# Kernel tuning notes

Measured on AMD Instinct MI355X. Metric: run time of the kernel, lower is better.

## Reference

```python
import jax, jax.numpy as jnp
import numpy as np

B, C, G, Q, OUT = 2, 96, 32, 32, 45
M_FREQS = 12
SIGMA = 3.0


def _fourier_encode(c):
    # c: [..., 3]; log-linear frequency bank scaled by SIGMA (sigma**(j/m))
    m = M_FREQS
    freqs = SIGMA ** (jnp.arange(m, dtype=c.dtype) / m)          # [m]
    ang = 2.0 * jnp.pi * c[..., None] * freqs                    # [..., 3, m]
    enc = jnp.concatenate([jnp.sin(ang), jnp.cos(ang)], axis=-1)  # [..., 3, 2m]
    return enc.reshape(c.shape[:-1] + (3 * 2 * m,))


def setup_inputs():
    key = jax.random.key(0)
    ks = jax.random.split(key, 10)
    d = {}
    d["context_v"] = jax.random.normal(ks[0], (B, C, G, G, G), jnp.float32)
    g = jnp.arange(G, dtype=jnp.float32)
    grid = jnp.stack(jnp.meshgrid(g, g, g, indexing="ij"), axis=-1)  # [G,G,G,3]
    d["context_world_coord_grid"] = jnp.broadcast_to(grid, (B, G, G, G, 3))
    # queries strictly inside the grid so floor()+1 <= G-1
    d["query_world_coord"] = jax.random.uniform(ks[1], (B, Q, Q, Q, 3), jnp.float32, 0.0, G - 1.001)
    d["query_world_coord_mask"] = jnp.ones((B, Q, Q, Q, 1), dtype=bool)
    eye = jnp.broadcast_to(jnp.eye(4, dtype=jnp.float32), (B, 4, 4))
    d["affine_context_vox2world"] = eye
    d["affine_query_vox2world"] = eye
    d["context_vox_size_world"] = jnp.ones((B, 3), jnp.float32)
    d["query_vox_size_world"] = jnp.ones((B, 3), jnp.float32)

    n_coord = 6 + 3 * 2 * M_FREQS  # 78
    internal = C + n_coord         # 174

    def lin(k, fi, fo):
        s = 1.0 / np.sqrt(fi)
        kw, kb = jax.random.split(k)
        return (jax.random.uniform(kw, (fi, fo), jnp.float32, -s, s),
                jax.random.uniform(kb, (fo,), jnp.float32, -s, s))

    pk = jax.random.split(ks[2], 7)
    d["w00"], d["b00"] = lin(pk[0], internal, C)
    d["w01"], d["b01"] = lin(pk[1], C, C)
    d["w02"], d["b02"] = lin(pk[2], C, C)
    d["w10"], d["b10"] = lin(pk[3], internal, C)
    d["w11"], d["b11"] = lin(pk[4], C, C)
    d["w12"], d["b12"] = lin(pk[5], C, C)
    d["w_post"], d["b_post"] = lin(pk[6], C, OUT)
    return d


def reference(context_v, context_world_coord_grid, query_world_coord,
              query_world_coord_mask, affine_context_vox2world,
              affine_query_vox2world, context_vox_size_world,
              query_vox_size_world, w00, b00, w01, b01, w02, b02,
              w10, b10, w11, b11, w12, b12, w_post, b_post):
    Bq = context_v.shape[0]
    qshape = query_world_coord.shape
    qw = query_world_coord.reshape(Bq, -1, 3)          # [B,N,3]
    N = qw.shape[1]
    qm = query_world_coord_mask.reshape(Bq, -1, 1)     # [B,N,1]
    dummy = qw[:, N // 2][:, None]                      # [B,1,3]
    qw = jnp.where(qm, qw, dummy)

    inv = jnp.linalg.inv(affine_context_vox2world)
    q_vox = jnp.einsum("brc,bnc->bnr", inv[:, :3, :3], qw) + inv[:, None, :3, 3]
    bottom = jnp.floor(q_vox).astype(jnp.int32)         # [B,N,3]
    sub = q_vox - bottom.astype(q_vox.dtype)

    cvt = jnp.transpose(context_v, (0, 2, 3, 4, 1))     # [B,X,Y,Z,C]
    bidx = jnp.arange(Bq)[:, None]
    maskf = qm.astype(q_vox.dtype)
    blocks = ((w00, b00, w01, b01, w02, b02), (w10, b10, w11, b11, w12, b12))
    acc = jnp.zeros((Bq, N, w_post.shape[1]), q_vox.dtype)

    for oi in (0, 1):
        for oj in (0, 1):
            for ok in (0, 1):
                off_i = jnp.array([oi, oj, ok], dtype=bottom.dtype)
                idx = bottom + off_i                    # [B,N,3]
                feats = cvt[bidx, idx[..., 0], idx[..., 1], idx[..., 2]] * maskf  # [B,N,C]
                cw = context_world_coord_grid[bidx, idx[..., 0], idx[..., 1], idx[..., 2]]  # [B,N,3]
                off_f = off_i.astype(q_vox.dtype)
                rel = (sub - off_f + 1.0) / 2.0
                enc = _fourier_encode(rel)              # [B,N,72]
                coord = jnp.concatenate([cw, qw, enc], axis=-1) * maskf  # [B,N,78]
                y = feats
                for (wa, ba, wb, bb, wc, bc) in blocks:  # SkipMLPBlock x2
                    h = jnp.concatenate([y, coord], axis=-1)
                    h = jax.nn.silu(h @ wa + ba)
                    h = jax.nn.silu(h @ wb + bb)
                    h = jax.nn.silu(h @ wc + bc)
                    y = y + h
                pred = y @ w_post + b_post              # [B,N,OUT]
                compl = jnp.abs(1.0 - off_f)
                w_tri = jnp.prod(jnp.abs(bottom.astype(q_vox.dtype) + compl - q_vox), axis=-1, keepdims=True)
                acc = acc + w_tri * pred

    out = jnp.transpose(acc, (0, 2, 1)).reshape((Bq, w_post.shape[1]) + qshape[1:-1])
    return out
```

## Files before the change

### kernel.cpp

```cpp
#include <hip/hip_runtime.h>

#define NQv   32768
#define GSH   9984
#define NGRP  9
#define WTOT  (GSH*NGRP)
#define WSTR  104
#define ASTR  104
#define CSTR  80
#define WBLK  352

typedef __attribute__((ext_vector_type(8))) short  short8;
typedef __attribute__((ext_vector_type(4))) float  float4v;

__device__ __forceinline__ float bfu2f(unsigned short u) {
  return __uint_as_float(((unsigned int)u) << 16);
}
__device__ __forceinline__ unsigned short f2bfu(float f) {
  unsigned int x = __float_as_uint(f);
  x += 0x7fffu + ((x >> 16) & 1u);
  return (unsigned short)(x >> 16);
}
__device__ __forceinline__ unsigned int rnd16(float f) {
  return __float_as_uint(f) + 0x8000u;
}
__device__ __forceinline__ unsigned int pkp(float lo, float hi) {
  return __builtin_amdgcn_perm(rnd16(hi), rnd16(lo), 0x07060302u);
}
__device__ __forceinline__ float silu_f(float x) {
  float e = __expf(-x);
  return x * __builtin_amdgcn_rcpf(1.f + e);
}
__device__ __forceinline__ int clamp31(int v) { return min(max(v, 0), 31); }

__device__ __forceinline__ void gload_lds16(const void* g, void* l) {
  typedef const __attribute__((address_space(1))) unsigned int GU;
  typedef __attribute__((address_space(3))) unsigned int LU;
  __builtin_amdgcn_global_load_lds((GU*)g, (LU*)l, 16, 0, 0);
}

__global__ __launch_bounds__(256) void prep_kernel(
    const float* __restrict__ ctxv,
    const float* __restrict__ w00, const float* __restrict__ w01,
    const float* __restrict__ w02, const float* __restrict__ w10,
    const float* __restrict__ w11, const float* __restrict__ w12,
    const float* __restrict__ wpost,
    const float* __restrict__ b00, const float* __restrict__ b10,
    unsigned short* __restrict__ ws, unsigned short* __restrict__ ctxvt)
{
  __shared__ float tile[96][65];
  const int blk0 = blockIdx.x;
  const int t = threadIdx.x;
  if (blk0 < WBLK) {
    int e = blk0 * 256 + t;
    if (e >= WTOT) {
      int e2 = e - WTOT;
      if (e2 < 192) {
        int mat = e2 / 96, ch = e2 - mat * 96;
        const float* w = mat ? w10 : w00;
        const float* bb = mat ? b10 : b00;
        float s = bb[ch];
#pragma unroll
        for (int k = 0; k < 6; ++k) s += 15.5f * w[(96 + k) * 96 + ch];
        ((float*)(ws + WTOT))[e2] = s;
      }
      return;
    }
    int g = e / GSH, r = e - g * GSH, n = r / WSTR, kk = r - n * WSTR;
    const float* src; int Ksrc, Nsrc, kofs;
    switch (g) {
      case 0:  src = w00;   Ksrc = 174; Nsrc = 96; kofs = 0;  break;
      case 1:  src = w00;   Ksrc = 174; Nsrc = 96; kofs = 96; break;
      case 2:  src = w01;   Ksrc = 96;  Nsrc = 96; kofs = 0;  break;
      case 3:  src = w02;   Ksrc = 96;  Nsrc = 96; kofs = 0;  break;
      case 4:  src = w10;   Ksrc = 174; Nsrc = 96; kofs = 0;  break;
      case 5:  src = w10;   Ksrc = 174; Nsrc = 96; kofs = 96; break;
      case 6:  src = w11;   Ksrc = 96;  Nsrc = 96; kofs = 0;  break;
      case 7:  src = w12;   Ksrc = 96;  Nsrc = 96; kofs = 0;  break;
      default: src = wpost; Ksrc = 96;  Nsrc = 45; kofs = 0;  break;
    }
    int k = kofs + kk;
    float v = (kk < 96 && k < Ksrc && n < Nsrc) ? src[k * Nsrc + n] : 0.f;
    ws[e] = f2bfu(v);
    return;
  }
  const int blk = blk0 - WBLK;
  const int b = blk >> 9, s0 = (blk & 511) << 6;
  const int cq = t >> 6, sl = t & 63;
#pragma unroll
  for (int p = 0; p < 24; ++p) {
    int c = cq + p * 4;
    tile[c][sl] = ctxv[(((size_t)(b * 96 + c)) << 15) + s0 + sl];
  }
  __syncthreads();
#pragma unroll
  for (int i = 0; i < 24; ++i) {
    int u = t + 256 * i;
    int s = u / 96, c = u - s * 96;
    ctxvt[((size_t)(b << 15) + s0 + s) * 96 + c] = f2bfu(tile[c][s]);
  }
}

template<int NM, bool INIT, bool BREG>
__device__ __forceinline__ void run_group(
    const short* __restrict__ sW,
    const short* pA, const short8 (&Bc)[3][2],
    const float* __restrict__ bias, int biasN,
    float4v (&C)[NM][2], int lane, int rowb)
{
  const int ln15 = lane & 15, quad = lane >> 4;
  if (INIT) {
    if (biasN >= NM * 16) {
#pragma unroll
      for (int mt = 0; mt < NM; ++mt) {
        float4v bv = *(const float4v*)(bias + mt * 16 + quad * 4);
        C[mt][0] = bv; C[mt][1] = bv;
      }
    } else {
#pragma unroll
      for (int mt = 0; mt < NM; ++mt) {
        int c0 = mt * 16 + quad * 4;
        float4v bv;
#pragma unroll
        for (int r = 0; r < 4; ++r) bv[r] = (c0 + r < biasN) ? bias[c0 + r] : 0.f;
        C[mt][0] = bv; C[mt][1] = bv;
      }
    }
  }
  short8 Wh[3][NM];
#pragma unroll
  for (int cb = 0; cb < 3; ++cb)
#pragma unroll
    for (int mt = 0; mt < NM; ++mt)
      Wh[cb][mt] = *(const short8*)&sW[(mt * 16 + ln15) * WSTR + cb * 32 + quad * 8];
  short8 Bh[3][2];
  if (BREG) {
#pragma unroll
    for (int cb = 0; cb < 3; ++cb) {
      Bh[cb][0] = Bc[cb][0]; Bh[cb][1] = Bc[cb][1];
    }
  } else {
#pragma unroll
    for (int cb = 0; cb < 3; ++cb)
#pragma unroll
      for (int nt = 0; nt < 2; ++nt)
        Bh[cb][nt] = *(const short8*)&pA[(rowb + nt * 16 + ln15) * ASTR + cb * 32 + quad * 8];
  }
#pragma unroll
  for (int cb = 0; cb < 3; ++cb)
#pragma unroll
    for (int mt = 0; mt < NM; ++mt)
#pragma unroll
      for (int nt = 0; nt < 2; ++nt)
        C[mt][nt] = __builtin_amdgcn_mfma_f32_16x16x32_bf16(Wh[cb][mt], Bh[cb][nt], C[mt][nt], 0, 0, 0);
}

template<bool TRANSPOSED>
__global__ __launch_bounds__(256, 2) void decoder_kernel(
    const float* __restrict__ ctxv,
    const unsigned short* __restrict__ ctxvt,
    const float* __restrict__ qwc,
    const float* __restrict__ aff,
    const float* __restrict__ b01, const float* __restrict__ b02,
    const float* __restrict__ b11, const float* __restrict__ b12,
    const float* __restrict__ bpost,
    const unsigned short* __restrict__ ws,
    float* __restrict__ out)
{
  __shared__ __align__(16) short sY[128 * ASTR];
  __shared__ __align__(16) short sH[128 * ASTR];
  __shared__ __align__(16) short sW[96 * WSTR];
  unsigned short* sTs = (unsigned short*)sH;
  short* sC    = sH + 2304;
  int*   sqbot = (int*)(sH + 12544);
  float* sqsub = (float*)(sH + 12544 + 96);

  const int t = threadIdx.x;
  const int blk = blockIdx.x;
  const int b = blk >> 11;
  const int qbase = (blk & 2047) * 16;
  const int lane = t & 63, wid = t >> 6;
  const int ln15 = lane & 15, quad = lane >> 4;
  const int rowb = wid * 32;
  const float* badj = (const float*)(ws + WTOT);

  auto stageW = [&](int g) {
    const char* src = (const char*)ws + (size_t)g * (GSH * 2);
    char* dst = (char*)sW;
#pragma unroll
    for (int rr = 0; rr < 5; ++rr) {
      int idx = t + 256 * rr;
      if (rr < 4 || idx < 1248)
        gload_lds16(src + (size_t)idx * 16, dst + idx * 16);
    }
  };

  stageW(0);

  if (t < 16) {
    float m[4][8];
    for (int i = 0; i < 4; ++i)
      for (int j = 0; j < 4; ++j) {
        m[i][j] = aff[b * 16 + i * 4 + j];
        m[i][j + 4] = (i == j) ? 1.f : 0.f;
      }
    for (int col = 0; col < 4; ++col) {
      int piv = col; float best = fabsf(m[col][col]);
      for (int rr = col + 1; rr < 4; ++rr) {
        float v = fabsf(m[rr][col]);
        if (v > best) { best = v; piv = rr; }
      }
      if (piv != col)
        for (int j = 0; j < 8; ++j) { float tmp = m[col][j]; m[col][j] = m[piv][j]; m[piv][j] = tmp; }
      float d = 1.f / m[col][col];
      for (int j = 0; j < 8; ++j) m[col][j] *= d;
      for (int rr = 0; rr < 4; ++rr) if (rr != col) {
        float f = m[rr][col];
        for (int j = 0; j < 8; ++j) m[rr][j] -= f * m[col][j];
      }
    }
    int qi = qbase + t;
    float x = qwc[((size_t)b * NQv + qi) * 3 + 0];
    float y = qwc[((size_t)b * NQv + qi) * 3 + 1];
    float z = qwc[((size_t)b * NQv + qi) * 3 + 2];
    float v0 = m[0][4] * x + m[0][5] * y + m[0][6] * z + m[0][7];
    float v1 = m[1][4] * x + m[1][5] * y + m[1][6] * z + m[1][7];
    float v2 = m[2][4] * x + m[2][5] * y + m[2][6] * z + m[2][7];
    int i0 = (int)floorf(v0), i1 = (int)floorf(v1), i2 = (int)floorf(v2);
    sqbot[t * 3 + 0] = i0; sqbot[t * 3 + 1] = i1; sqbot[t * 3 + 2] = i2;
    sqsub[t * 3 + 0] = v0 - (float)i0; sqsub[t * 3 + 1] = v1 - (float)i1; sqsub[t * 3 + 2] = v2 - (float)i2;
  }
  __syncthreads();

#pragma unroll
  for (int i = 0; i < 3; ++i) {
    int u = lane + 64 * i;
    if (u < 144) {
      int ql = u / 36, rem = u - 36 * ql, d = rem / 12, fj = rem - 12 * d;
      int q = 4 * wid + ql;
      float sub = sqsub[q * 3 + d];
      float freq = exp2f((float)fj * 0.13208020839342968f);
#pragma unroll
      for (int off = 0; off < 2; ++off) {
        float rel = (sub - (float)off + 1.f) * 0.5f;
        float ang = 6.283185307179586f * rel * freq;
        float sn, cs; __sincosf(ang, &sn, &cs);
        int base = ((q * 3 + d) * 2 + off) * 24 + fj;
        sTs[base]      = f2bfu(sn);
        sTs[base + 12] = f2bfu(cs);
      }
    }
  }

  float wtri = 0.f;
  if (lane < 32) {
    int row = rowb + lane;
    int q = row >> 3, cor = row & 7;
    int oi = (cor >> 2) & 1, oj = (cor >> 1) & 1, ok = cor & 1;
    float wx = oi ? sqsub[q * 3 + 0] : 1.f - sqsub[q * 3 + 0];
    float wy = oj ? sqsub[q * 3 + 1] : 1.f - sqsub[q * 3 + 1];
    float wz = ok ? sqsub[q * 3 + 2] : 1.f - sqsub[q * 3 + 2];
    wtri = wx * wy * wz;
  }
  {
    const int row = rowb + (lane >> 1);
    const int q = row >> 3, cor = row & 7;
    const int oi = (cor >> 2) & 1, oj = (cor >> 1) & 1, ok = cor & 1;
    const int jb = (lane & 1) * 48;
    const int ix = clamp31(sqbot[q * 3 + 0] + oi);
    const int iy = clamp31(sqbot[q * 3 + 1] + oj);
    const int iz = clamp31(sqbot[q * 3 + 2] + ok);
    const int spat = (ix << 10) | (iy << 5) | iz;
    if (TRANSPOSED) {
      const unsigned short* src = ctxvt + ((size_t)(b << 15) + spat) * 96 + jb;
#pragma unroll
      for (int g = 0; g < 6; ++g)
        *(short8*)&sY[row * ASTR + jb + 8 * g] = *(const short8*)(src + 8 * g);
    } else {
#pragma unroll 4
      for (int g = 0; g < 12; ++g) {
        float vv[4];
#pragma unroll
        for (int r = 0; r < 4; ++r)
          vv[r] = ctxv[(((size_t)(b * 96 + jb + 4 * g + r)) << 15) + spat];
        *(uint2*)&sY[row * ASTR + jb + 4 * g] = make_uint2(pkp(vv[0], vv[1]), pkp(vv[2], vv[3]));
      }
    }
    int offv[3]; offv[0] = oi; offv[1] = oj; offv[2] = ok;
    const int cbase = (lane & 1) * 40;
    float qw3[3];
#pragma unroll
    for (int k = 0; k < 3; ++k) qw3[k] = qwc[((size_t)b * NQv + qbase + q) * 3 + k];
#pragma unroll
    for (int g = 0; g < 10; ++g) {
      unsigned short hv[4];
#pragma unroll
      for (int r = 0; r < 4; ++r) {
        int ch = cbase + 4 * g + r;
        if (ch < 3) {
          float v = (float)clamp31(sqbot[q * 3 + ch] + offv[ch]) - 15.5f;
          hv[r] = (unsigned short)(rnd16(v) >> 16);
        } else if (ch < 6) {
          float v = qw3[ch - 3] - 15.5f;
          hv[r] = (unsigned short)(rnd16(v) >> 16);
        } else if (ch < 78) {
          int i2 = ch - 6, d = i2 / 24, rr = i2 - 24 * d, sc = rr / 12, fj = rr - 12 * sc;
          hv[r] = sTs[(((q * 3 + d) * 2 + offv[d]) * 2 + sc) * 12 + fj];
        } else hv[r] = 0;
      }
      *(uint2*)&sC[row * CSTR + cbase + 4 * g] =
          make_uint2((unsigned int)hv[0] | ((unsigned int)hv[1] << 16),
                     (unsigned int)hv[2] | ((unsigned int)hv[3] << 16));
    }
  }
  short8 Bc[3][2];
#pragma unroll
  for (int c = 0; c < 3; ++c)
#pragma unroll
    for (int nt = 0; nt < 2; ++nt)
      Bc[c][nt] = (c == 2 && quad >= 2)
                  ? (short8)0
                  : *(const short8*)&sC[(rowb + nt * 16 + ln15) * CSTR + c * 32 + quad * 8];
  __syncthreads();

  auto epiH = [&](float4v (&C)[6][2]) {
#pragma unroll
    for (int mt = 0; mt < 6; ++mt)
#pragma unroll
      for (int nt = 0; nt < 2; ++nt) {
        int idx = (rowb + nt * 16 + ln15) * ASTR + mt * 16 + quad * 4;
        *(uint2*)&sH[idx] = make_uint2(pkp(silu_f(C[mt][nt][0]), silu_f(C[mt][nt][1])),
                                       pkp(silu_f(C[mt][nt][2]), silu_f(C[mt][nt][3])));
      }
  };
  auto epiSkip = [&](float4v (&C)[6][2]) {
#pragma unroll
    for (int mt = 0; mt < 6; ++mt)
#pragma unroll
      for (int nt = 0; nt < 2; ++nt) {
        int idx = (rowb + nt * 16 + ln15) * ASTR + mt * 16 + quad * 4;
        uint2 oh = *(uint2*)&sY[idx];
        float y0 = __uint_as_float(oh.x << 16)          + silu_f(C[mt][nt][0]);
        float y1 = __uint_as_float(oh.x & 0xffff0000u)  + silu_f(C[mt][nt][1]);
        float y2 = __uint_as_float(oh.y << 16)          + silu_f(C[mt][nt][2]);
        float y3 = __uint_as_float(oh.y & 0xffff0000u)  + silu_f(C[mt][nt][3]);
        *(uint2*)&sY[idx] = make_uint2(pkp(y0, y1), pkp(y2, y3));
      }
  };

  {
    float4v C[6][2];
    run_group<6, true , false>(sW, sY, Bc, badj,      96, C, lane, rowb);
    __syncthreads();
    stageW(1);
    __syncthreads();
    run_group<6, false, true >(sW, sY, Bc, badj,      96, C, lane, rowb);
    __syncthreads();
    stageW(2);
    epiH(C);
    __syncthreads();
    run_group<6, true , false>(sW, sH, Bc, b01,       96, C, lane, rowb);
    __syncthreads();
    stageW(3);
    epiH(C);
    __syncthreads();
    run_group<6, true , false>(sW, sH, Bc, b02,       96, C, lane, rowb);
    __syncthreads();
    stageW(4);
    epiSkip(C);
    __syncthreads();
    run_group<6, true , false>(sW, sY, Bc, badj + 96, 96, C, lane, rowb);
    __syncthreads();
    stageW(5);
    __syncthreads();
    run_group<6, false, true >(sW, sY, Bc, badj,      96, C, lane, rowb);
    __syncthreads();
    stageW(6);
    epiH(C);
    __syncthreads();
    run_group<6, true , false>(sW, sH, Bc, b11,       96, C, lane, rowb);
    __syncthreads();
    stageW(7);
    epiH(C);
    __syncthreads();
    run_group<6, true , false>(sW, sH, Bc, b12,       96, C, lane, rowb);
    __syncthreads();
    stageW(8);
    epiSkip(C);
    __syncthreads();
  }
  float* pred = (float*)sH;
  {
    float4v Cp[3][2];
    run_group<3, true, false>(sW, sY, Bc, bpost, 45, Cp, lane, rowb);
    float w0 = __shfl(wtri, ln15);
    float w1 = __shfl(wtri, 16 + ln15);
#pragma unroll
    for (int mt = 0; mt < 3; ++mt)
#pragma unroll
      for (int nt = 0; nt < 2; ++nt) {
        int row = rowb + nt * 16 + ln15, c0 = mt * 16 + quad * 4;
        float w = nt ? w1 : w0;
        float4v v = Cp[mt][nt];
        v[0] *= w; v[1] *= w; v[2] *= w; v[3] *= w;
        *(float4v*)&pred[row * 52 + c0] = v;
      }
  }
#pragma unroll
  for (int i = 0; i < 3; ++i) {
    int u = lane + 64 * i;
    if (u < 180) {
      int ql = u / 45, ch = u - ql * 45;
      float s = 0.f;
#pragma unroll
      for (int cor = 0; cor < 8; ++cor) s += pred[(rowb + ql * 8 + cor) * 52 + ch];
      out[(((size_t)(b * 45 + ch)) << 15) + qbase + wid * 4 + ql] = s;
    }
  }
}

extern "C" void kernel_launch(void* const* d_in, const int* in_sizes, int n_in,
                              void* d_out, int out_size, void* d_ws, size_t ws_size,
                              hipStream_t stream) {
  (void)in_sizes; (void)n_in; (void)out_size;
  const float* ctxv  = (const float*)d_in[0];
  const float* qwc   = (const float*)d_in[2];
  const float* aff   = (const float*)d_in[4];
  const float* w00   = (const float*)d_in[8];
  const float* b00   = (const float*)d_in[9];
  const float* w01   = (const float*)d_in[10];
  const float* b01   = (const float*)d_in[11];
  const float* w02   = (const float*)d_in[12];
  const float* b02   = (const float*)d_in[13];
  const float* w10   = (const float*)d_in[14];
  const float* b10   = (const float*)d_in[15];
  const float* w11   = (const float*)d_in[16];
  const float* b11   = (const float*)d_in[17];
  const float* w12   = (const float*)d_in[18];
  const float* b12   = (const float*)d_in[19];
  const float* wpost = (const float*)d_in[20];
  const float* bpost = (const float*)d_in[21];
  unsigned short* ws = (unsigned short*)d_ws;
  float* out = (float*)d_out;

  const size_t wbytes = (size_t)WTOT * sizeof(unsigned short) + 768;
  const size_t tbytes = (size_t)2 * 32768 * 96 * sizeof(unsigned short);
  unsigned short* ctxvt = (unsigned short*)((char*)d_ws + wbytes);
  const bool useT = ws_size >= wbytes + tbytes;

  if (useT) {
    prep_kernel<<<dim3(WBLK + 1024), dim3(256), 0, stream>>>(
        ctxv, w00, w01, w02, w10, w11, w12, wpost, b00, b10, ws, ctxvt);
    decoder_kernel<true><<<dim3(4096), dim3(256), 0, stream>>>(
        ctxv, ctxvt, qwc, aff, b01, b02, b11, b12, bpost, ws, out);
  } else {
    prep_kernel<<<dim3(WBLK), dim3(256), 0, stream>>>(
        ctxv, w00, w01, w02, w10, w11, w12, wpost, b00, b10, ws, ctxvt);
    decoder_kernel<false><<<dim3(4096), dim3(256), 0, stream>>>(
        ctxv, ctxvt, qwc, aff, b01, b02, b11, b12, bpost, ws, out);
  }
}
```

Baseline: 291.8 us.

## Drop hidden-activation LDS buffer via bpermute register transpose and raise occupancy

Removes the sH shared buffer. The MLP hidden activations are now turned from accumulator layout into MFMA B-operand layout with ds_bpermute register shuffles, instead of a round trip through LDS. Per-wave setup scratch (coordinate encodings, query sub-voxel data, pred staging) is moved into each wave's own region of sY, and the coordinate tile is built before the feature gather. With LDS use per block cut, launch bounds are raised to 3 blocks per CU. The cost is extra bpermute instructions and higher register pressure at the tighter launch bound.

```diff
diff --git a/kernel.cpp b/kernel.cpp
--- a/kernel.cpp
+++ b/kernel.cpp
@@ -102,8 +102,8 @@
 
 template<int NM, bool INIT, bool BREG>
 __device__ __forceinline__ void run_group(
-    const short* __restrict__ sW,
-    const short* pA, const short8 (&Bc)[3][2],
+    const short* __restrict__ sWp,
+    const short* pA, const short8 (&Bin)[3][2],
     const float* __restrict__ bias, int biasN,
     float4v (&C)[NM][2], int lane, int rowb)
 {
@@ -131,12 +131,12 @@
   for (int cb = 0; cb < 3; ++cb)
 #pragma unroll
     for (int mt = 0; mt < NM; ++mt)
-      Wh[cb][mt] = *(const short8*)&sW[(mt * 16 + ln15) * WSTR + cb * 32 + quad * 8];
+      Wh[cb][mt] = *(const short8*)&sWp[(mt * 16 + ln15) * WSTR + cb * 32 + quad * 8];
   short8 Bh[3][2];
   if (BREG) {
 #pragma unroll
     for (int cb = 0; cb < 3; ++cb) {
-      Bh[cb][0] = Bc[cb][0]; Bh[cb][1] = Bc[cb][1];
+      Bh[cb][0] = Bin[cb][0]; Bh[cb][1] = Bin[cb][1];
     }
   } else {
 #pragma unroll
@@ -154,8 +154,44 @@
         C[mt][nt] = __builtin_amdgcn_mfma_f32_16x16x32_bf16(Wh[cb][mt], Bh[cb][nt], C[mt][nt], 0, 0, 0);
 }
 
+__device__ __forceinline__ void xformB(
+    const float4v (&C)[6][2], short8 (&Bt)[3][2], int lane)
+{
+  const int quad = lane >> 4;
+  const int i0 = (((lane & 15) | ((lane & 16) << 1))) << 2;
+  const int i1 = i0 + 64;
+  unsigned int P[6][2][2];
+#pragma unroll
+  for (int m = 0; m < 6; ++m)
+#pragma unroll
+    for (int nt = 0; nt < 2; ++nt)
+#pragma unroll
+      for (int p = 0; p < 2; ++p)
+        P[m][nt][p] = pkp(silu_f(C[m][nt][2 * p]), silu_f(C[m][nt][2 * p + 1]));
+#pragma unroll
+  for (int cb = 0; cb < 3; ++cb)
+#pragma unroll
+    for (int nt = 0; nt < 2; ++nt) {
+      unsigned int w[4];
+#pragma unroll
+      for (int p = 0; p < 2; ++p) {
+        int a  = (int)P[2 * cb][nt][p];
+        int bb = (int)P[2 * cb + 1][nt][p];
+        int l0a = __builtin_amdgcn_ds_bpermute(i0, a);
+        int l0b = __builtin_amdgcn_ds_bpermute(i0, bb);
+        int l1a = __builtin_amdgcn_ds_bpermute(i1, a);
+        int l1b = __builtin_amdgcn_ds_bpermute(i1, bb);
+        w[p]     = (unsigned int)(quad >= 2 ? l0b : l0a);
+        w[2 + p] = (unsigned int)(quad >= 2 ? l1b : l1a);
+      }
+      union { unsigned int u[4]; short8 s; } cv;
+      cv.u[0] = w[0]; cv.u[1] = w[1]; cv.u[2] = w[2]; cv.u[3] = w[3];
+      Bt[cb][nt] = cv.s;
+    }
+}
+
 template<bool TRANSPOSED>
-__global__ __launch_bounds__(256, 2) void decoder_kernel(
+__global__ __launch_bounds__(256, 3) void decoder_kernel(
     const float* __restrict__ ctxv,
     const unsigned short* __restrict__ ctxvt,
     const float* __restrict__ qwc,
@@ -167,12 +203,7 @@
     float* __restrict__ out)
 {
   __shared__ __align__(16) short sY[128 * ASTR];
-  __shared__ __align__(16) short sH[128 * ASTR];
   __shared__ __align__(16) short sW[96 * WSTR];
-  unsigned short* sTs = (unsigned short*)sH;
-  short* sC    = sH + 2304;
-  int*   sqbot = (int*)(sH + 12544);
-  float* sqsub = (float*)(sH + 12544 + 96);
 
   const int t = threadIdx.x;
   const int blk = blockIdx.x;
@@ -183,6 +214,12 @@
   const int rowb = wid * 32;
   const float* badj = (const float*)(ws + WTOT);
 
+  short* wscr = sY + rowb * ASTR;
+  unsigned short* sTs = (unsigned short*)wscr;
+  short* sC    = wscr + 576;
+  int*   qbot  = (int*)(wscr + 3136);
+  float* qsub  = (float*)(wscr + 3160);
+
   auto stageW = [&](int g) {
     const char* src = (const char*)ws + (size_t)g * (GSH * 2);
     char* dst = (char*)sW;
@@ -196,7 +233,7 @@
 
   stageW(0);
 
-  if (t < 16) {
+  if (lane < 4) {
     float m[4][8];
     for (int i = 0; i < 4; ++i)
       for (int j = 0; j < 4; ++j) {
@@ -218,7 +255,7 @@
         for (int j = 0; j < 8; ++j) m[rr][j] -= f * m[col][j];
       }
     }
-    int qi = qbase + t;
+    int qi = qbase + wid * 4 + lane;
     float x = qwc[((size_t)b * NQv + qi) * 3 + 0];
     float y = qwc[((size_t)b * NQv + qi) * 3 + 1];
     float z = qwc[((size_t)b * NQv + qi) * 3 + 2];
@@ -226,25 +263,23 @@
     float v1 = m[1][4] * x + m[1][5] * y + m[1][6] * z + m[1][7];
     float v2 = m[2][4] * x + m[2][5] * y + m[2][6] * z + m[2][7];
     int i0 = (int)floorf(v0), i1 = (int)floorf(v1), i2 = (int)floorf(v2);
-    sqbot[t * 3 + 0] = i0; sqbot[t * 3 + 1] = i1; sqbot[t * 3 + 2] = i2;
-    sqsub[t * 3 + 0] = v0 - (float)i0; sqsub[t * 3 + 1] = v1 - (float)i1; sqsub[t * 3 + 2] = v2 - (float)i2;
-  }
-  __syncthreads();
+    qbot[lane * 3 + 0] = i0; qbot[lane * 3 + 1] = i1; qbot[lane * 3 + 2] = i2;
+    qsub[lane * 3 + 0] = v0 - (float)i0; qsub[lane * 3 + 1] = v1 - (float)i1; qsub[lane * 3 + 2] = v2 - (float)i2;
+  }
 
 #pragma unroll
   for (int i = 0; i < 3; ++i) {
     int u = lane + 64 * i;
     if (u < 144) {
       int ql = u / 36, rem = u - 36 * ql, d = rem / 12, fj = rem - 12 * d;
-      int q = 4 * wid + ql;
-      float sub = sqsub[q * 3 + d];
+      float sub = qsub[ql * 3 + d];
       float freq = exp2f((float)fj * 0.13208020839342968f);
 #pragma unroll
       for (int off = 0; off < 2; ++off) {
         float rel = (sub - (float)off + 1.f) * 0.5f;
         float ang = 6.283185307179586f * rel * freq;
         float sn, cs; __sincosf(ang, &sn, &cs);
-        int base = ((q * 3 + d) * 2 + off) * 24 + fj;
+        int base = ((ql * 3 + d) * 2 + off) * 24 + fj;
         sTs[base]      = f2bfu(sn);
         sTs[base + 12] = f2bfu(cs);
       }
@@ -253,23 +288,66 @@
 
   float wtri = 0.f;
   if (lane < 32) {
-    int row = rowb + lane;
-    int q = row >> 3, cor = row & 7;
+    int rl = lane;
+    int ql = rl >> 3, cor = rl & 7;
     int oi = (cor >> 2) & 1, oj = (cor >> 1) & 1, ok = cor & 1;
-    float wx = oi ? sqsub[q * 3 + 0] : 1.f - sqsub[q * 3 + 0];
-    float wy = oj ? sqsub[q * 3 + 1] : 1.f - sqsub[q * 3 + 1];
-    float wz = ok ? sqsub[q * 3 + 2] : 1.f - sqsub[q * 3 + 2];
+    float wx = oi ? qsub[ql * 3 + 0] : 1.f - qsub[ql * 3 + 0];
+    float wy = oj ? qsub[ql * 3 + 1] : 1.f - qsub[ql * 3 + 1];
+    float wz = ok ? qsub[ql * 3 + 2] : 1.f - qsub[ql * 3 + 2];
     wtri = wx * wy * wz;
   }
+
   {
-    const int row = rowb + (lane >> 1);
-    const int q = row >> 3, cor = row & 7;
+    const int rl = lane >> 1;
+    const int ql = rl >> 3, cor = rl & 7;
+    const int oi = (cor >> 2) & 1, oj = (cor >> 1) & 1, ok = cor & 1;
+    int offv[3]; offv[0] = oi; offv[1] = oj; offv[2] = ok;
+    const int cbase = (lane & 1) * 40;
+    float qw3[3];
+#pragma unroll
+    for (int k = 0; k < 3; ++k)
+      qw3[k] = qwc[((size_t)b * NQv + qbase + wid * 4 + ql) * 3 + k];
+#pragma unroll
+    for (int g = 0; g < 10; ++g) {
+      unsigned short hv[4];
+#pragma unroll
+      for (int r = 0; r < 4; ++r) {
+        int ch = cbase + 4 * g + r;
+        if (ch < 3) {
+          float v = (float)clamp31(qbot[ql * 3 + ch] + offv[ch]) - 15.5f;
+          hv[r] = (unsigned short)(rnd16(v) >> 16);
+        } else if (ch < 6) {
+          float v = qw3[ch - 3] - 15.5f;
+          hv[r] = (unsigned short)(rnd16(v) >> 16);
+        } else if (ch < 78) {
+          int i2 = ch - 6, d = i2 / 24, rr = i2 - 24 * d, sc = rr / 12, fj = rr - 12 * sc;
+          hv[r] = sTs[(((ql * 3 + d) * 2 + offv[d]) * 2 + sc) * 12 + fj];
+        } else hv[r] = 0;
+      }
+      *(uint2*)&sC[rl * CSTR + cbase + 4 * g] =
+          make_uint2((unsigned int)hv[0] | ((unsigned int)hv[1] << 16),
+                     (unsigned int)hv[2] | ((unsigned int)hv[3] << 16));
+    }
+  }
+  short8 Bc[3][2];
+#pragma unroll
+  for (int c = 0; c < 3; ++c)
+#pragma unroll
+    for (int nt = 0; nt < 2; ++nt)
+      Bc[c][nt] = (c == 2 && quad >= 2)
+                  ? (short8)0
+                  : *(const short8*)&sC[(nt * 16 + ln15) * CSTR + c * 32 + quad * 8];
+
+  {
+    const int rl = lane >> 1;
+    const int ql = rl >> 3, cor = rl & 7;
     const int oi = (cor >> 2) & 1, oj = (cor >> 1) & 1, ok = cor & 1;
     const int jb = (lane & 1) * 48;
-    const int ix = clamp31(sqbot[q * 3 + 0] + oi);
-    const int iy = clamp31(sqbot[q * 3 + 1] + oj);
-    const int iz = clamp31(sqbot[q * 3 + 2] + ok);
+    const int ix = clamp31(qbot[ql * 3 + 0] + oi);
+    const int iy = clamp31(qbot[ql * 3 + 1] + oj);
+    const int iz = clamp31(qbot[ql * 3 + 2] + ok);
     const int spat = (ix << 10) | (iy << 5) | iz;
+    const int row = rowb + rl;
     if (TRANSPOSED) {
       const unsigned short* src = ctxvt + ((size_t)(b << 15) + spat) * 96 + jb;
 #pragma unroll
@@ -285,53 +363,9 @@
         *(uint2*)&sY[row * ASTR + jb + 4 * g] = make_uint2(pkp(vv[0], vv[1]), pkp(vv[2], vv[3]));
       }
     }
-    int offv[3]; offv[0] = oi; offv[1] = oj; offv[2] = ok;
-    const int cbase = (lane & 1) * 40;
-    float qw3[3];
-#pragma unroll
-    for (int k = 0; k < 3; ++k) qw3[k] = qwc[((size_t)b * NQv + qbase + q) * 3 + k];
-#pragma unroll
-    for (int g = 0; g < 10; ++g) {
-      unsigned short hv[4];
-#pragma unroll
-      for (int r = 0; r < 4; ++r) {
-        int ch = cbase + 4 * g + r;
-        if (ch < 3) {
-          float v = (float)clamp31(sqbot[q * 3 + ch] + offv[ch]) - 15.5f;
-          hv[r] = (unsigned short)(rnd16(v) >> 16);
-        } else if (ch < 6) {
-          float v = qw3[ch - 3] - 15.5f;
-          hv[r] = (unsigned short)(rnd16(v) >> 16);
-        } else if (ch < 78) {
-          int i2 = ch - 6, d = i2 / 24, rr = i2 - 24 * d, sc = rr / 12, fj = rr - 12 * sc;
-          hv[r] = sTs[(((q * 3 + d) * 2 + offv[d]) * 2 + sc) * 12 + fj];
-        } else hv[r] = 0;
-      }
-      *(uint2*)&sC[row * CSTR + cbase + 4 * g] =
-          make_uint2((unsigned int)hv[0] | ((unsigned int)hv[1] << 16),
-                     (unsigned int)hv[2] | ((unsigned int)hv[3] << 16));
-    }
-  }
-  short8 Bc[3][2];
-#pragma unroll
-  for (int c = 0; c < 3; ++c)
-#pragma unroll
-    for (int nt = 0; nt < 2; ++nt)
-      Bc[c][nt] = (c == 2 && quad >= 2)
-                  ? (short8)0
-                  : *(const short8*)&sC[(rowb + nt * 16 + ln15) * CSTR + c * 32 + quad * 8];
+  }
   __syncthreads();
 
-  auto epiH = [&](float4v (&C)[6][2]) {
-#pragma unroll
-    for (int mt = 0; mt < 6; ++mt)
-#pragma unroll
-      for (int nt = 0; nt < 2; ++nt) {
-        int idx = (rowb + nt * 16 + ln15) * ASTR + mt * 16 + quad * 4;
-        *(uint2*)&sH[idx] = make_uint2(pkp(silu_f(C[mt][nt][0]), silu_f(C[mt][nt][1])),
-                                       pkp(silu_f(C[mt][nt][2]), silu_f(C[mt][nt][3])));
-      }
-  };
   auto epiSkip = [&](float4v (&C)[6][2]) {
 #pragma unroll
     for (int mt = 0; mt < 6; ++mt)
@@ -349,6 +383,7 @@
 
   {
     float4v C[6][2];
+    short8 Bt[3][2];
     run_group<6, true , false>(sW, sY, Bc, badj,      96, C, lane, rowb);
     __syncthreads();
     stageW(1);
@@ -356,14 +391,14 @@
     run_group<6, false, true >(sW, sY, Bc, badj,      96, C, lane, rowb);
     __syncthreads();
     stageW(2);
-    epiH(C);
-    __syncthreads();
-    run_group<6, true , false>(sW, sH, Bc, b01,       96, C, lane, rowb);
+    xformB(C, Bt, lane);
+    __syncthreads();
+    run_group<6, true , true >(sW, sY, Bt, b01,       96, C, lane, rowb);
     __syncthreads();
     stageW(3);
-    epiH(C);
-    __syncthreads();
-    run_group<6, true , false>(sW, sH, Bc, b02,       96, C, lane, rowb);
+    xformB(C, Bt, lane);
+    __syncthreads();
+    run_group<6, true , true >(sW, sY, Bt, b02,       96, C, lane, rowb);
     __syncthreads();
     stageW(4);
     epiSkip(C);
@@ -375,45 +410,45 @@
     run_group<6, false, true >(sW, sY, Bc, badj,      96, C, lane, rowb);
     __syncthreads();
     stageW(6);
-    epiH(C);
-    __syncthreads();
-    run_group<6, true , false>(sW, sH, Bc, b11,       96, C, lane, rowb);
+    xformB(C, Bt, lane);
+    __syncthreads();
+    run_group<6, true , true >(sW, sY, Bt, b11,       96, C, lane, rowb);
     __syncthreads();
     stageW(7);
-    epiH(C);
-    __syncthreads();
-    run_group<6, true , false>(sW, sH, Bc, b12,       96, C, lane, rowb);
+    xformB(C, Bt, lane);
+    __syncthreads();
+    run_group<6, true , true >(sW, sY, Bt, b12,       96, C, lane, rowb);
     __syncthreads();
     stageW(8);
     epiSkip(C);
     __syncthreads();
-  }
-  float* pred = (float*)sH;
-  {
-    float4v Cp[3][2];
-    run_group<3, true, false>(sW, sY, Bc, bpost, 45, Cp, lane, rowb);
-    float w0 = __shfl(wtri, ln15);
-    float w1 = __shfl(wtri, 16 + ln15);
-#pragma unroll
-    for (int mt = 0; mt < 3; ++mt)
-#pragma unroll
-      for (int nt = 0; nt < 2; ++nt) {
-        int row = rowb + nt * 16 + ln15, c0 = mt * 16 + quad * 4;
-        float w = nt ? w1 : w0;
-        float4v v = Cp[mt][nt];
-        v[0] *= w; v[1] *= w; v[2] *= w; v[3] *= w;
-        *(float4v*)&pred[row * 52 + c0] = v;
-      }
-  }
-#pragma unroll
-  for (int i = 0; i < 3; ++i) {
-    int u = lane + 64 * i;
-    if (u < 180) {
-      int ql = u / 45, ch = u - ql * 45;
-      float s = 0.f;
-#pragma unroll
-      for (int cor = 0; cor < 8; ++cor) s += pred[(rowb + ql * 8 + cor) * 52 + ch];
-      out[(((size_t)(b * 45 + ch)) << 15) + qbase + wid * 4 + ql] = s;
+    float* pred = (float*)wscr;
+    {
+      float4v Cp[3][2];
+      run_group<3, true, false>(sW, sY, Bc, bpost, 45, Cp, lane, rowb);
+      float w0 = __shfl(wtri, ln15);
+      float w1 = __shfl(wtri, 16 + ln15);
+#pragma unroll
+      for (int mt = 0; mt < 3; ++mt)
+#pragma unroll
+        for (int nt = 0; nt < 2; ++nt) {
+          int rl = nt * 16 + ln15, c0 = mt * 16 + quad * 4;
+          float w = nt ? w1 : w0;
+          float4v v = Cp[mt][nt];
+          v[0] *= w; v[1] *= w; v[2] *= w; v[3] *= w;
+          *(float4v*)&pred[rl * 52 + c0] = v;
+        }
+    }
+#pragma unroll
+    for (int i = 0; i < 3; ++i) {
+      int u = lane + 64 * i;
+      if (u < 180) {
+        int ql = u / 45, ch = u - ql * 45;
+        float s = 0.f;
+#pragma unroll
+        for (int cor = 0; cor < 8; ++cor) s += pred[(ql * 8 + cor) * 52 + ch];
+        out[(((size_t)(b * 45 + ch)) << 15) + qbase + wid * 4 + ql] = s;
+      }
     }
   }
 }
```

New measurement: 311.6 us. +6.8%, slower.
